# Optimization experiments

Hardware: AMD Instinct MI355X
Metric: run time of the kernel (lower is better)

## Reference

```python
import jax, jax.numpy as jnp
import numpy as np

B, S, D, H, DH = 2, 4096, 768, 12, 64

def setup_inputs() -> dict:
    key = jax.random.key(0)
    kx, kq, kk, kv = jax.random.split(key, 4)
    x = jax.random.normal(kx, (B, S, D), dtype=jnp.float32)
    # per-head Q/K/V projection weights, stacked over heads: [H, d_in, d_out]
    Wq = jax.random.normal(kq, (H, D, DH), dtype=jnp.float32) * 0.02
    Wk = jax.random.normal(kk, (H, D, DH), dtype=jnp.float32) * 0.02
    Wv = jax.random.normal(kv, (H, D, DH), dtype=jnp.float32) * 0.02
    return {"x": x, "Wq": Wq, "Wk": Wk, "Wv": Wv}

def reference(x, Wq, Wk, Wv):
    b, s, _ = x.shape
    # per-head linear projections (qkv_bias=False), batched over heads
    q = jnp.einsum('bsd,hde->bhse', x, Wq)  # [B,H,S,DH]
    k = jnp.einsum('bsd,hde->bhse', x, Wk)
    v = jnp.einsum('bsd,hde->bhse', x, Wv)
    scale = 1.0 / jnp.sqrt(jnp.asarray(q.shape[-1], q.dtype))
    scores = jnp.einsum('bhqe,bhke->bhqk', q, k) * scale  # [B,H,S,S]
    causal_mask = jnp.triu(jnp.ones((s, s), dtype=bool), k=1)
    scores = jnp.where(causal_mask, -jnp.inf, scores)
    attn = jax.nn.softmax(scores, axis=-1)  # dropout p=0 -> identity
    ctx = jnp.einsum('bhqk,bhke->bhqe', attn, v)  # [B,H,S,DH]
    # concat heads on last dim (matches torch.cat of per-head outputs)
    return ctx.transpose(0, 2, 1, 3).reshape(b, s, -1)  # [B,S,H*DH]
```

## Files before the change

### kernel.cpp

```cpp
#include <hip/hip_runtime.h>
#include <hip/hip_bf16.h>
#include <stdint.h>

#define B_  2
#define S_  4096
#define D_  768
#define H_  12
#define DH_ 64
#define BS_ (B_*S_)

typedef __bf16 bf16x8 __attribute__((ext_vector_type(8)));
typedef short  svec8  __attribute__((ext_vector_type(8)));
typedef float  fvec4  __attribute__((ext_vector_type(4)));
typedef int    ivec4  __attribute__((ext_vector_type(4)));
typedef unsigned short ushort_t;

__device__ __forceinline__ ushort_t bfc(float f){
    return __builtin_bit_cast(ushort_t, (__bf16)f);
}

__device__ __forceinline__ unsigned cvt_pk_bf16(float lo, float hi){
    unsigned r;
    asm("v_cvt_pk_bf16_f32 %0, %1, %2" : "=v"(r) : "v"(lo), "v"(hi));
    return r;
}

__device__ __forceinline__ fvec4 mfma16(svec8 a, svec8 b, fvec4 c){
    return __builtin_amdgcn_mfma_f32_16x16x32_bf16(
        __builtin_bit_cast(bf16x8, a), __builtin_bit_cast(bf16x8, b), c, 0, 0, 0);
}

__global__ __launch_bounds__(256) void prep(
    const float* __restrict__ X,
    const float* __restrict__ Wq, const float* __restrict__ Wk, const float* __restrict__ Wv,
    ushort_t* __restrict__ Xb, ushort_t* __restrict__ Wsz)
{
    const int bid = blockIdx.x;
    if (bid < 3072) {
        size_t idx = ((size_t)bid * 256 + threadIdx.x) * 8;
        float4 d0 = *(const float4*)(X + idx);
        float4 d1 = *(const float4*)(X + idx + 4);
        bf16x8 pk;
        pk[0] = (__bf16)d0.x; pk[1] = (__bf16)d0.y;
        pk[2] = (__bf16)d0.z; pk[3] = (__bf16)d0.w;
        pk[4] = (__bf16)d1.x; pk[5] = (__bf16)d1.y;
        pk[6] = (__bf16)d1.z; pk[7] = (__bf16)d1.w;
        *(svec8*)(Xb + idx) = __builtin_bit_cast(svec8, pk);
    } else {
        const int v  = bid - 3072;
        const int wt = v % 3;
        const int hk = v / 3;
        const int h  = hk / 12, kt = hk % 12;
        const float* W  = (wt == 0) ? Wq : (wt == 1) ? Wk : Wv;
        const float* Wh = W + (size_t)h * (D_ * DH_) + (size_t)kt * 64 * DH_;
        ushort_t* dst = Wsz + (size_t)(hk * 3 + wt) * 4096;
        #pragma unroll
        for (int i = 0; i < 2; i++) {
            int a    = (threadIdx.x + 256 * i) * 8;
            int k5   = a >> 11;
            int nblk = (a >> 9) & 3;
            int n    = nblk * 16 + ((a >> 5) & 15);
            int q2   = (a >> 3) & 3;
            int k0   = k5 * 32 + q2 * 8;
            bf16x8 pk;
            #pragma unroll
            for (int j = 0; j < 8; j++) pk[j] = (__bf16)Wh[(k0 + j) * DH_ + n];
            *(svec8*)(dst + a) = __builtin_bit_cast(svec8, pk);
        }
    }
}

__global__ __launch_bounds__(256, 3) void qkv_proj(
    const ushort_t* __restrict__ Xb, const ushort_t* __restrict__ Wsz,
    ushort_t* __restrict__ Qb, ushort_t* __restrict__ Kb, ushort_t* __restrict__ Vg)
{
    const int m0 = blockIdx.x * 128;
    const int h  = blockIdx.y;

    __shared__ ushort_t smem[64 * 136];
    ushort_t* Xs  = smem;
    ushort_t* XsT = smem;

    const int tid  = threadIdx.x;
    const int w    = tid >> 6;
    const int lane = tid & 63;
    const int quad = lane >> 4;
    const int l15  = lane & 15;
    const int lp8  = (l15 * 4 + quad) * 8;

    fvec4 acc[3][2][4];
    #pragma unroll
    for (int wt = 0; wt < 3; wt++)
        #pragma unroll
        for (int i = 0; i < 2; i++)
            #pragma unroll
            for (int j = 0; j < 4; j++) acc[wt][i][j] = (fvec4){0.f, 0.f, 0.f, 0.f};

    const ushort_t* xsrc = Xb + (size_t)m0 * D_;
    const ushort_t* wsrc = Wsz + (size_t)(h * 12) * 3 * 4096 + lp8;

    int xr[4], xdu[4];
    #pragma unroll
    for (int i = 0; i < 4; i++) {
        int v = tid + 256 * i;
        int r = v >> 3, t = v & 7;
        xr[i]  = r * D_ + t * 8;
        xdu[i] = (((r >> 4) * 2 + (t >> 2)) * 64 + (r & 15) * 4 + (t & 3)) * 8;
    }

    svec8 xd[4];
    #pragma unroll
    for (int i = 0; i < 4; i++) xd[i] = *(const svec8*)(xsrc + xr[i]);

    for (int kt = 0; kt < 12; kt++) {
        #pragma unroll
        for (int i = 0; i < 4; i++) *(svec8*)(Xs + xdu[i]) = xd[i];
        __syncthreads();

        if (kt < 11) {
            #pragma unroll
            for (int i = 0; i < 4; i++)
                xd[i] = *(const svec8*)(xsrc + xr[i] + (kt + 1) * 64);
        }

        const ushort_t* wp = wsrc + (size_t)kt * 3 * 4096;
        #pragma unroll
        for (int ks = 0; ks < 2; ks++) {
            svec8 a0 = *(const svec8*)(Xs + (4 * w + ks) * 512 + lp8);
            svec8 a1 = *(const svec8*)(Xs + (4 * w + 2 + ks) * 512 + lp8);
            #pragma unroll
            for (int wt = 0; wt < 3; wt++) {
                svec8 wb[4];
                #pragma unroll
                for (int ns = 0; ns < 4; ns++)
                    wb[ns] = *(const svec8*)(wp + (wt * 8 + ks * 4 + ns) * 512);
                #pragma unroll
                for (int ns = 0; ns < 4; ns++) {
                    acc[wt][0][ns] = mfma16(a0, wb[ns], acc[wt][0][ns]);
                    acc[wt][1][ns] = mfma16(a1, wb[ns], acc[wt][1][ns]);
                }
            }
        }
        __syncthreads();
    }

    const float qs = 0.18033688011112042f;
    #pragma unroll
    for (int ms = 0; ms < 2; ms++)
        #pragma unroll
        for (int ns = 0; ns < 4; ns++)
            #pragma unroll
            for (int r = 0; r < 4; r++) {
                int row = m0 + 32 * w + ms * 16 + quad * 4 + r;
                int col = h * DH_ + ns * 16 + l15;
                Qb[(size_t)row * D_ + col] = bfc(acc[0][ms][ns][r] * qs);
                Kb[(size_t)row * D_ + col] = bfc(acc[1][ms][ns][r]);
            }
    #pragma unroll
    for (int ms = 0; ms < 2; ms++)
        #pragma unroll
        for (int ns = 0; ns < 4; ns++)
            #pragma unroll
            for (int r = 0; r < 4; r++) {
                int sl = 32 * w + ms * 16 + quad * 4 + r;
                int e  = ns * 16 + l15;
                XsT[e * 136 + sl] = bfc(acc[2][ms][ns][r]);
            }
    __syncthreads();
    #pragma unroll
    for (int i = 0; i < 4; i++) {
        int v = tid + 256 * i;
        int e = v >> 4, s0 = (v & 15) * 8;
        svec8 d = *(const svec8*)(XsT + e * 136 + s0);
        *(svec8*)(Vg + (size_t)(h * DH_ + e) * BS_ + m0 + s0) = d;
    }
}

__global__ __launch_bounds__(256, 6) void attn(
    const ushort_t* __restrict__ Qb, const ushort_t* __restrict__ Kb,
    const ushort_t* __restrict__ Vg, float* __restrict__ Out)
{
    const int fid = blockIdx.x;
    const int g   = fid & 255;
    const int r6  = fid >> 8;
    const int gl  = g & 63;
    const int gh  = g >> 6;
    const int hb  = gh * 6 + r6;
    const int h   = hb % H_;
    const int b   = hb / H_;
    const int offs = (r6 >> 1 == 0) ? 0 : (r6 >> 1 == 1) ? 21 : 43;
    const int base = (gl + offs) & 63;
    const int qt   = (r6 & 1) ? 63 - base : base;
    const int q0 = qt * 64;

    const int tid  = threadIdx.x;
    const int w    = tid >> 6;
    const int lane = tid & 63;
    const int quad = lane >> 4;
    const int l15  = lane & 15;

    __shared__ ushort_t Ks[64 * 72];
    __shared__ ushort_t Vt[64 * 72];

    const size_t hboff = (size_t)b * S_ * D_ + (size_t)h * DH_;
    const ushort_t* Vh = Vg + (size_t)h * DH_ * BS_ + (size_t)b * S_;

    const int sr = tid >> 3;
    const int sc = (tid & 7) * 8;
    const int pr0 = (((sr      >> 2) & 1) << 5) | (((sr      >> 5) & 1) << 4) |
                    (((sr      >> 4) & 1) << 3) | (((sr      >> 3) & 1) << 2) | (sr & 3);
    const int sr1 = sr + 32;
    const int pr1 = (((sr1 >> 2) & 1) << 5) | (((sr1 >> 5) & 1) << 4) |
                    (((sr1 >> 4) & 1) << 3) | (((sr1 >> 3) & 1) << 2) | (sr1 & 3);

    svec8 aq[2];
    {
        const ushort_t* qrow = Qb + hboff + (size_t)(q0 + 16 * w + l15) * D_;
        aq[0] = *(const svec8*)(qrow + quad * 8);
        aq[1] = *(const svec8*)(qrow + 32 + quad * 8);
    }

    float ls  = 0.f;
    fvec4 acc[4];
    #pragma unroll
    for (int n = 0; n < 4; n++) acc[n] = (fvec4){0.f, 0.f, 0.f, 0.f};

    const ushort_t* kp = Kb + hboff + (size_t)sr * D_ + sc;
    const ushort_t* vp = Vh + (size_t)sr * BS_ + sc;

    svec8 kd[2], vd[2];
    kd[0] = *(const svec8*)(kp);
    kd[1] = *(const svec8*)(kp + (size_t)32 * D_);
    vd[0] = *(const svec8*)(vp);
    vd[1] = *(const svec8*)(vp + (size_t)32 * BS_);
    kp += (size_t)64 * D_;
    vp += 64;
    *(svec8*)(Ks + pr0 * 72 + sc) = kd[0];
    *(svec8*)(Ks + pr1 * 72 + sc) = kd[1];
    *(svec8*)(Vt + sr  * 72 + sc) = vd[0];
    *(svec8*)(Vt + sr1 * 72 + sc) = vd[1];

    for (int kt = 0; kt <= qt; ++kt) {
        __syncthreads();

        if (kt < qt) {
            kd[0] = *(const svec8*)(kp);
            kd[1] = *(const svec8*)(kp + (size_t)32 * D_);
            vd[0] = *(const svec8*)(vp);
            vd[1] = *(const svec8*)(vp + (size_t)32 * BS_);
            kp += (size_t)64 * D_;
            vp += 64;
        }

        fvec4 st[4];
        #pragma unroll
        for (int n = 0; n < 4; n++) st[n] = (fvec4){0.f, 0.f, 0.f, 0.f};
        #pragma unroll
        for (int ks = 0; ks < 2; ks++)
            #pragma unroll
            for (int n = 0; n < 4; n++) {
                svec8 ka = *(const svec8*)(Ks + (n * 16 + l15) * 72 + ks * 32 + quad * 8);
                st[n] = mfma16(ka, aq[ks], st[n]);
            }

        if (kt == qt) {
            #pragma unroll
            for (int n = 0; n < 4; n++)
                #pragma unroll
                for (int r = 0; r < 4; r++) {
                    int key = (n & 1) * 32 + quad * 8 + (n >> 1) * 4 + r;
                    int row = 16 * w + l15;
                    if (key > row) st[n][r] = -INFINITY;
                }
        }

        ivec4 ai0, ai1;
        float psum[4];
        #pragma unroll
        for (int n = 0; n < 4; n++) {
            float p0 = exp2f(st[n][0]);
            float p1 = exp2f(st[n][1]);
            float p2 = exp2f(st[n][2]);
            float p3 = exp2f(st[n][3]);
            psum[n] = (p0 + p1) + (p2 + p3);
            unsigned d0 = cvt_pk_bf16(p0, p1);
            unsigned d1 = cvt_pk_bf16(p2, p3);
            if (n == 0)      { ai0[0] = (int)d0; ai0[1] = (int)d1; }
            else if (n == 1) { ai1[0] = (int)d0; ai1[1] = (int)d1; }
            else if (n == 2) { ai0[2] = (int)d0; ai0[3] = (int)d1; }
            else             { ai1[2] = (int)d0; ai1[3] = (int)d1; }
        }
        ls += (psum[0] + psum[2]) + (psum[1] + psum[3]);
        svec8 ap0 = __builtin_bit_cast(svec8, ai0);
        svec8 ap1 = __builtin_bit_cast(svec8, ai1);

        #pragma unroll
        for (int ks = 0; ks < 2; ks++) {
            svec8 ap = ks ? ap1 : ap0;
            #pragma unroll
            for (int n = 0; n < 4; n++) {
                svec8 bv = *(const svec8*)(Vt + (n * 16 + l15) * 72 + ks * 32 + quad * 8);
                acc[n] = mfma16(ap, bv, acc[n]);
            }
        }

        __syncthreads();

        if (kt < qt) {
            *(svec8*)(Ks + pr0 * 72 + sc) = kd[0];
            *(svec8*)(Ks + pr1 * 72 + sc) = kd[1];
            *(svec8*)(Vt + sr  * 72 + sc) = vd[0];
            *(svec8*)(Vt + sr1 * 72 + sc) = vd[1];
        }
    }

    float lsum = ls;
    lsum += __shfl_xor(lsum, 16);
    lsum += __shfl_xor(lsum, 32);
    float li[4];
    #pragma unroll
    for (int r = 0; r < 4; r++)
        li[r] = __shfl(lsum, quad * 16 + quad * 4 + r);
    #pragma unroll
    for (int n = 0; n < 4; n++)
        #pragma unroll
        for (int r = 0; r < 4; r++) {
            int row = q0 + 16 * w + quad * 4 + r;
            int col = h * DH_ + n * 16 + l15;
            Out[((size_t)b * S_ + row) * D_ + col] = acc[n][r] / li[r];
        }
}

extern "C" void kernel_launch(void* const* d_in, const int* in_sizes, int n_in,
                              void* d_out, int out_size, void* d_ws, size_t ws_size,
                              hipStream_t stream)
{
    const float* X  = (const float*)d_in[0];
    const float* Wq = (const float*)d_in[1];
    const float* Wk = (const float*)d_in[2];
    const float* Wv = (const float*)d_in[3];

    ushort_t* Qb = (ushort_t*)d_ws;
    ushort_t* Kb = Qb + (size_t)BS_ * D_;
    ushort_t* Vg = Kb + (size_t)BS_ * D_;

    ushort_t* Xb  = (ushort_t*)d_out;
    ushort_t* Wsz = Xb + (size_t)BS_ * D_;
    float* Out = (float*)d_out;

    prep<<<dim3(3072 + 432), dim3(256), 0, stream>>>(X, Wq, Wk, Wv, Xb, Wsz);
    qkv_proj<<<dim3(64, H_), dim3(256), 0, stream>>>(Xb, Wsz, Qb, Kb, Vg);
    attn<<<dim3((S_ / 64) * H_ * B_), dim3(256), 0, stream>>>(Qb, Kb, Vg, Out);
}
```

Measured before the change: 247.1 us.

## Rewrite attention inner loop with 32x32 MFMA and split-K waves

New measurement: 239.0 us. -3.3%, faster.

```diff
diff --git a/kernel.cpp b/kernel.cpp
--- a/kernel.cpp
+++ b/kernel.cpp
@@ -12,6 +12,7 @@
 typedef __bf16 bf16x8 __attribute__((ext_vector_type(8)));
 typedef short  svec8  __attribute__((ext_vector_type(8)));
 typedef float  fvec4  __attribute__((ext_vector_type(4)));
+typedef float  fvec16 __attribute__((ext_vector_type(16)));
 typedef int    ivec4  __attribute__((ext_vector_type(4)));
 typedef unsigned short ushort_t;
 
@@ -25,8 +26,17 @@
     return r;
 }
 
+__device__ __forceinline__ void perm32swap(unsigned &a, unsigned &b){
+    asm volatile("v_permlane32_swap_b32 %0, %1" : "+v"(a), "+v"(b));
+}
+
 __device__ __forceinline__ fvec4 mfma16(svec8 a, svec8 b, fvec4 c){
     return __builtin_amdgcn_mfma_f32_16x16x32_bf16(
+        __builtin_bit_cast(bf16x8, a), __builtin_bit_cast(bf16x8, b), c, 0, 0, 0);
+}
+
+__device__ __forceinline__ fvec16 mfma32(svec8 a, svec8 b, fvec16 c){
+    return __builtin_amdgcn_mfma_f32_32x32x16_bf16(
         __builtin_bit_cast(bf16x8, a), __builtin_bit_cast(bf16x8, b), c, 0, 0, 0);
 }
 
@@ -176,159 +186,178 @@
     }
 }
 
-__global__ __launch_bounds__(256, 6) void attn(
+__global__ __launch_bounds__(256, 4) void attn(
     const ushort_t* __restrict__ Qb, const ushort_t* __restrict__ Kb,
     const ushort_t* __restrict__ Vg, float* __restrict__ Out)
 {
     const int fid = blockIdx.x;
-    const int g   = fid & 255;
-    const int r6  = fid >> 8;
-    const int gl  = g & 63;
-    const int gh  = g >> 6;
-    const int hb  = gh * 6 + r6;
-    const int h   = hb % H_;
-    const int b   = hb / H_;
-    const int offs = (r6 >> 1 == 0) ? 0 : (r6 >> 1 == 1) ? 21 : 43;
-    const int base = (gl + offs) & 63;
-    const int qt   = (r6 & 1) ? 63 - base : base;
-    const int q0 = qt * 64;
+    const int qt  = (S_ / 64 - 1) - fid / (H_ * B_);
+    const int r24 = fid % (H_ * B_);
+    const int h   = r24 % H_;
+    const int b   = r24 / H_;
+    const int q0  = qt * 64;
 
     const int tid  = threadIdx.x;
     const int w    = tid >> 6;
+    const int qh   = w >> 1;
+    const int kh   = w & 1;
     const int lane = tid & 63;
-    const int quad = lane >> 4;
-    const int l15  = lane & 15;
-
-    __shared__ ushort_t Ks[64 * 72];
-    __shared__ ushort_t Vt[64 * 72];
+    const int l31  = lane & 31;
+    const int lhi  = lane >> 5;
+
+    __shared__ ushort_t Ksm[4096];
+    __shared__ ushort_t Vsm[4096];
+    __shared__ float    LsX[128];
 
     const size_t hboff = (size_t)b * S_ * D_ + (size_t)h * DH_;
     const ushort_t* Vh = Vg + (size_t)h * DH_ * BS_ + (size_t)b * S_;
 
-    const int sr = tid >> 3;
-    const int sc = (tid & 7) * 8;
-    const int pr0 = (((sr      >> 2) & 1) << 5) | (((sr      >> 5) & 1) << 4) |
-                    (((sr      >> 4) & 1) << 3) | (((sr      >> 3) & 1) << 2) | (sr & 3);
-    const int sr1 = sr + 32;
-    const int pr1 = (((sr1 >> 2) & 1) << 5) | (((sr1 >> 5) & 1) << 4) |
-                    (((sr1 >> 4) & 1) << 3) | (((sr1 >> 3) & 1) << 2) | (sr1 & 3);
-
-    svec8 aq[2];
+    const int sr  = tid >> 3;
+    const int scc = tid & 7;
+    const int sta0 = ((scc >> 1)) * 512 + (sr & 31) * 16 + (scc & 1) * 8;
+    const int sta1 = (4 + (scc >> 1)) * 512 + (sr & 31) * 16 + (scc & 1) * 8;
+
+    svec8 qf[4];
     {
-        const ushort_t* qrow = Qb + hboff + (size_t)(q0 + 16 * w + l15) * D_;
-        aq[0] = *(const svec8*)(qrow + quad * 8);
-        aq[1] = *(const svec8*)(qrow + 32 + quad * 8);
-    }
-
-    float ls  = 0.f;
-    fvec4 acc[4];
-    #pragma unroll
-    for (int n = 0; n < 4; n++) acc[n] = (fvec4){0.f, 0.f, 0.f, 0.f};
-
-    const ushort_t* kp = Kb + hboff + (size_t)sr * D_ + sc;
-    const ushort_t* vp = Vh + (size_t)sr * BS_ + sc;
-
-    svec8 kd[2], vd[2];
-    kd[0] = *(const svec8*)(kp);
-    kd[1] = *(const svec8*)(kp + (size_t)32 * D_);
-    vd[0] = *(const svec8*)(vp);
-    vd[1] = *(const svec8*)(vp + (size_t)32 * BS_);
+        const ushort_t* qrow = Qb + hboff + (size_t)(q0 + qh * 32 + l31) * D_ + lhi * 8;
+        qf[0] = *(const svec8*)(qrow);
+        qf[1] = *(const svec8*)(qrow + 16);
+        qf[2] = *(const svec8*)(qrow + 32);
+        qf[3] = *(const svec8*)(qrow + 48);
+    }
+
+    const int loffA = l31 * 16 + lhi * 8;
+
+    float ls = 0.f;
+    fvec16 acc0, acc1;
+    #pragma unroll
+    for (int r = 0; r < 16; r++) { acc0[r] = 0.f; acc1[r] = 0.f; }
+
+    const ushort_t* kp = Kb + hboff + (size_t)sr * D_ + scc * 8;
+    const ushort_t* vp = Vh + (size_t)sr * BS_ + scc * 8;
+
+    svec8 kd0, kd1, vd0, vd1;
+    kd0 = *(const svec8*)(kp);
+    kd1 = *(const svec8*)(kp + (size_t)32 * D_);
+    vd0 = *(const svec8*)(vp);
+    vd1 = *(const svec8*)(vp + (size_t)32 * BS_);
     kp += (size_t)64 * D_;
     vp += 64;
-    *(svec8*)(Ks + pr0 * 72 + sc) = kd[0];
-    *(svec8*)(Ks + pr1 * 72 + sc) = kd[1];
-    *(svec8*)(Vt + sr  * 72 + sc) = vd[0];
-    *(svec8*)(Vt + sr1 * 72 + sc) = vd[1];
+    *(svec8*)(Ksm + sta0) = kd0;
+    *(svec8*)(Ksm + sta1) = kd1;
+    *(svec8*)(Vsm + sta0) = vd0;
+    *(svec8*)(Vsm + sta1) = vd1;
 
     for (int kt = 0; kt <= qt; ++kt) {
         __syncthreads();
 
         if (kt < qt) {
-            kd[0] = *(const svec8*)(kp);
-            kd[1] = *(const svec8*)(kp + (size_t)32 * D_);
-            vd[0] = *(const svec8*)(vp);
-            vd[1] = *(const svec8*)(vp + (size_t)32 * BS_);
+            kd0 = *(const svec8*)(kp);
+            kd1 = *(const svec8*)(kp + (size_t)32 * D_);
+            vd0 = *(const svec8*)(vp);
+            vd1 = *(const svec8*)(vp + (size_t)32 * BS_);
             kp += (size_t)64 * D_;
             vp += 64;
         }
 
-        fvec4 st[4];
-        #pragma unroll
-        for (int n = 0; n < 4; n++) st[n] = (fvec4){0.f, 0.f, 0.f, 0.f};
-        #pragma unroll
-        for (int ks = 0; ks < 2; ks++)
-            #pragma unroll
-            for (int n = 0; n < 4; n++) {
-                svec8 ka = *(const svec8*)(Ks + (n * 16 + l15) * 72 + ks * 32 + quad * 8);
-                st[n] = mfma16(ka, aq[ks], st[n]);
-            }
+        fvec16 st;
+        #pragma unroll
+        for (int r = 0; r < 16; r++) st[r] = 0.f;
+        #pragma unroll
+        for (int s = 0; s < 4; s++) {
+            svec8 ka = *(const svec8*)(Ksm + (kh * 4 + s) * 512 + loffA);
+            st = mfma32(ka, qf[s], st);
+        }
 
         if (kt == qt) {
             #pragma unroll
-            for (int n = 0; n < 4; n++)
-                #pragma unroll
-                for (int r = 0; r < 4; r++) {
-                    int key = (n & 1) * 32 + quad * 8 + (n >> 1) * 4 + r;
-                    int row = 16 * w + l15;
-                    if (key > row) st[n][r] = -INFINITY;
-                }
-        }
-
-        ivec4 ai0, ai1;
-        float psum[4];
-        #pragma unroll
-        for (int n = 0; n < 4; n++) {
-            float p0 = exp2f(st[n][0]);
-            float p1 = exp2f(st[n][1]);
-            float p2 = exp2f(st[n][2]);
-            float p3 = exp2f(st[n][3]);
-            psum[n] = (p0 + p1) + (p2 + p3);
-            unsigned d0 = cvt_pk_bf16(p0, p1);
-            unsigned d1 = cvt_pk_bf16(p2, p3);
-            if (n == 0)      { ai0[0] = (int)d0; ai0[1] = (int)d1; }
-            else if (n == 1) { ai1[0] = (int)d0; ai1[1] = (int)d1; }
-            else if (n == 2) { ai0[2] = (int)d0; ai0[3] = (int)d1; }
-            else             { ai1[2] = (int)d0; ai1[3] = (int)d1; }
-        }
-        ls += (psum[0] + psum[2]) + (psum[1] + psum[3]);
-        svec8 ap0 = __builtin_bit_cast(svec8, ai0);
-        svec8 ap1 = __builtin_bit_cast(svec8, ai1);
-
-        #pragma unroll
-        for (int ks = 0; ks < 2; ks++) {
-            svec8 ap = ks ? ap1 : ap0;
-            #pragma unroll
-            for (int n = 0; n < 4; n++) {
-                svec8 bv = *(const svec8*)(Vt + (n * 16 + l15) * 72 + ks * 32 + quad * 8);
-                acc[n] = mfma16(ap, bv, acc[n]);
-            }
+            for (int r = 0; r < 16; r++) {
+                int key_in = kh * 32 + (r & 3) + 8 * (r >> 2) + 4 * lhi;
+                int qloc   = qh * 32 + l31;
+                if (key_in > qloc) st[r] = -INFINITY;
+            }
+        }
+
+        float p[16];
+        #pragma unroll
+        for (int r = 0; r < 16; r++) p[r] = exp2f(st[r]);
+        ls += (((p[0] + p[1]) + (p[2] + p[3])) + ((p[4] + p[5]) + (p[6] + p[7])))
+            + (((p[8] + p[9]) + (p[10] + p[11])) + ((p[12] + p[13]) + (p[14] + p[15])));
+
+        unsigned a0 = cvt_pk_bf16(p[0], p[1]),   a1 = cvt_pk_bf16(p[4], p[5]);
+        perm32swap(a0, a1);
+        unsigned b0 = cvt_pk_bf16(p[2], p[3]),   b1 = cvt_pk_bf16(p[6], p[7]);
+        perm32swap(b0, b1);
+        unsigned c0 = cvt_pk_bf16(p[8], p[9]),   c1 = cvt_pk_bf16(p[12], p[13]);
+        perm32swap(c0, c1);
+        unsigned d0 = cvt_pk_bf16(p[10], p[11]), d1 = cvt_pk_bf16(p[14], p[15]);
+        perm32swap(d0, d1);
+        ivec4 w0 = { (int)a0, (int)b0, (int)a1, (int)b1 };
+        ivec4 w1 = { (int)c0, (int)d0, (int)c1, (int)d1 };
+        svec8 pb0 = __builtin_bit_cast(svec8, w0);
+        svec8 pb1 = __builtin_bit_cast(svec8, w1);
+
+        #pragma unroll
+        for (int s2 = 0; s2 < 2; s2++) {
+            svec8 pb = s2 ? pb1 : pb0;
+            svec8 va0 = *(const svec8*)(Vsm + (0 + kh * 2 + s2) * 512 + loffA);
+            svec8 va1 = *(const svec8*)(Vsm + (4 + kh * 2 + s2) * 512 + loffA);
+            acc0 = mfma32(va0, pb, acc0);
+            acc1 = mfma32(va1, pb, acc1);
         }
 
         __syncthreads();
 
         if (kt < qt) {
-            *(svec8*)(Ks + pr0 * 72 + sc) = kd[0];
-            *(svec8*)(Ks + pr1 * 72 + sc) = kd[1];
-            *(svec8*)(Vt + sr  * 72 + sc) = vd[0];
-            *(svec8*)(Vt + sr1 * 72 + sc) = vd[1];
-        }
-    }
-
-    float lsum = ls;
-    lsum += __shfl_xor(lsum, 16);
-    lsum += __shfl_xor(lsum, 32);
-    float li[4];
-    #pragma unroll
-    for (int r = 0; r < 4; r++)
-        li[r] = __shfl(lsum, quad * 16 + quad * 4 + r);
-    #pragma unroll
-    for (int n = 0; n < 4; n++)
-        #pragma unroll
-        for (int r = 0; r < 4; r++) {
-            int row = q0 + 16 * w + quad * 4 + r;
-            int col = h * DH_ + n * 16 + l15;
-            Out[((size_t)b * S_ + row) * D_ + col] = acc[n][r] / li[r];
-        }
+            *(svec8*)(Ksm + sta0) = kd0;
+            *(svec8*)(Ksm + sta1) = kd1;
+            *(svec8*)(Vsm + sta0) = vd0;
+            *(svec8*)(Vsm + sta1) = vd1;
+        }
+    }
+
+    if (kh == 1) {
+        float* dst = (qh == 0) ? (float*)Ksm : (float*)Vsm;
+        #pragma unroll
+        for (int cix = 0; cix < 8; cix++) {
+            int rq = cix & 3;
+            fvec4 v4;
+            #pragma unroll
+            for (int j = 0; j < 4; j++)
+                v4[j] = (cix < 4) ? acc0[rq * 4 + j] : acc1[rq * 4 + j];
+            *(fvec4*)(dst + cix * 256 + lane * 4) = v4;
+        }
+        LsX[qh * 64 + lane] = ls;
+    }
+    __syncthreads();
+    if (kh == 0) {
+        const float* src = (qh == 0) ? (const float*)Ksm : (const float*)Vsm;
+        #pragma unroll
+        for (int cix = 0; cix < 8; cix++) {
+            int rq = cix & 3;
+            fvec4 v4 = *(const fvec4*)(src + cix * 256 + lane * 4);
+            #pragma unroll
+            for (int j = 0; j < 4; j++) {
+                if (cix < 4) acc0[rq * 4 + j] += v4[j];
+                else         acc1[rq * 4 + j] += v4[j];
+            }
+        }
+        float lsc = ls + LsX[qh * 64 + lane];
+        lsc += __shfl_xor(lsc, 32);
+        float inv = 1.f / lsc;
+        const int row = q0 + qh * 32 + l31;
+        float* orow = Out + ((size_t)b * S_ + row) * D_ + h * DH_;
+        #pragma unroll
+        for (int cix = 0; cix < 8; cix++) {
+            int eg = cix >> 2, rq = cix & 3;
+            int colb = eg * 32 + 8 * rq + 4 * lhi;
+            fvec4 o;
+            #pragma unroll
+            for (int j = 0; j < 4; j++)
+                o[j] = ((cix < 4) ? acc0[rq * 4 + j] : acc1[rq * 4 + j]) * inv;
+            *(fvec4*)(orow + colb) = o;
+        }
+    }
 }
 
 extern "C" void kernel_launch(void* const* d_in, const int* in_sizes, int n_in,
```
